# Optimization experiments

Hardware: AMD Instinct MI355X
Metric: run time of the kernel (lower is better)

The kernel has to match this reference:

```python
import jax, jax.numpy as jnp
import numpy as np

V, NB, NJ, NP, NK = 6890, 10, 24, 207, 19
PARENTS = np.array([-1, 0, 0, 0, 1, 2, 3, 4, 5, 6, 7, 8, 9, 9, 9, 12, 13, 14, 16, 17, 18, 19, 20, 21])


def setup_inputs():
    key = jax.random.key(0)
    ks = jax.random.split(key, 9)
    B = 1024
    beta = jax.random.normal(ks[0], (B, NB), jnp.float32)
    theta = jax.random.normal(ks[1], (B, NJ * 3), jnp.float32) * 0.3  # axis-angle per joint
    trans = jax.random.normal(ks[2], (B, 3), jnp.float32)
    v_template = jax.random.normal(ks[3], (V, 3), jnp.float32)
    shapedirs = jax.random.normal(ks[4], (NB, V * 3), jnp.float32) * 0.03
    Jr = jax.random.uniform(ks[5], (V, NJ), jnp.float32)
    J_regressor = Jr / jnp.sum(Jr, axis=0, keepdims=True)
    posedirs = jax.random.normal(ks[6], (NP, V * 3), jnp.float32) * 0.01
    jr = jax.random.uniform(ks[7], (V, NK), jnp.float32)
    joint_regressor = jr / jnp.sum(jr, axis=0, keepdims=True)
    w = jax.random.uniform(ks[8], (V, NJ), jnp.float32)
    weights = w / jnp.sum(w, axis=1, keepdims=True)  # LBS weights, rows sum to 1
    return dict(beta=beta, theta=theta, trans=trans, v_template=v_template,
                shapedirs=shapedirs, J_regressor=J_regressor, posedirs=posedirs,
                joint_regressor=joint_regressor, weights=weights)


def batch_rodrigues(theta):
    # theta: (N,3) axis-angle -> (N,3,3) rotation matrices via quaternions (HMR-style)
    angle = jnp.linalg.norm(theta + 1e-8, axis=1, keepdims=True)
    half = angle * 0.5
    v = (theta / angle) * jnp.sin(half)
    quat = jnp.concatenate([jnp.cos(half), v], axis=1)
    quat = quat / jnp.linalg.norm(quat, axis=1, keepdims=True)
    w, x, y, z = quat[:, 0], quat[:, 1], quat[:, 2], quat[:, 3]
    rot = jnp.stack([
        1 - 2 * (y * y + z * z), 2 * (x * y - w * z), 2 * (x * z + w * y),
        2 * (x * y + w * z), 1 - 2 * (x * x + z * z), 2 * (y * z - w * x),
        2 * (x * z - w * y), 2 * (y * z + w * x), 1 - 2 * (x * x + y * y)], axis=1)
    return rot.reshape(-1, 3, 3)


def batch_global_rigid_transformation(Rs, J):
    # Rs: (B,24,3,3), J: (B,24,3); rotate_base=True
    B = Rs.shape[0]
    rot_x = jnp.array([[1., 0., 0.], [0., -1., 0.], [0., 0., -1.]], jnp.float32)
    root_R = Rs[:, 0] @ rot_x

    def make_A(R, t):  # (B,3,3),(B,3) -> (B,4,4)
        top = jnp.concatenate([R, t[:, :, None]], axis=2)
        bot = jnp.broadcast_to(jnp.array([0., 0., 0., 1.], jnp.float32), (B, 1, 4))
        return jnp.concatenate([top, bot], axis=1)

    results = [make_A(root_R, J[:, 0])]
    for i in range(1, NJ):  # fixed 24-joint kinematic chain
        t = J[:, i] - J[:, PARENTS[i]]
        results.append(results[PARENTS[i]] @ make_A(Rs[:, i], t))
    res = jnp.stack(results, axis=1)  # (B,24,4,4)
    new_J = res[:, :, :3, 3]
    j_w0 = jnp.concatenate([J, jnp.zeros_like(J[:, :, :1])], axis=2)  # (B,24,4), homo w=0
    init_bone = jnp.einsum('bjrc,bjc->bjr', res, j_w0)
    A = res.at[:, :, :, 3].add(-init_bone)  # subtract only last column (matches F.pad trick)
    return new_J, A


def reference(beta, theta, trans, v_template, shapedirs, J_regressor, posedirs, joint_regressor, weights):
    B = beta.shape[0]
    v_shaped = (beta @ shapedirs).reshape(B, V, 3) + v_template
    J = jnp.einsum('bvc,vj->bjc', v_shaped, J_regressor)  # (B,24,3)
    Rs = batch_rodrigues(theta.reshape(-1, 3)).reshape(B, NJ, 3, 3)
    pose_feature = (Rs[:, 1:] - jnp.eye(3, dtype=Rs.dtype)).reshape(B, NP)
    v_posed = (pose_feature @ posedirs).reshape(B, V, 3) + v_shaped
    _, A = batch_global_rigid_transformation(Rs, J)
    T = jnp.einsum('vj,bjrc->bvrc', weights, A)  # (B,V,4,4) per-vertex skinning transforms
    homo = jnp.concatenate([v_posed, jnp.ones((B, V, 1), v_posed.dtype)], axis=2)
    verts = jnp.einsum('bvrc,bvc->bvr', T, homo)[:, :, :3] + trans[:, None, :]
    joints = jnp.einsum('bvc,vk->bkc', verts, joint_regressor)  # (B,19,3)
    return joints
```

## Files before the change

kernel.cpp:

```cpp
#include <hip/hip_runtime.h>
#include <hip/hip_bf16.h>

constexpr int Vn   = 6890;
constexpr int VC3  = 20670;
constexpr int NKB  = 216;
constexpr int QT   = 224;
constexpr int NMG  = 14;
constexpr int NCOL = 480;
constexpr int MC   = 1368;
constexpr int KCH  = 27;

using bf16x8  = __attribute__((ext_vector_type(8))) short;
using floatx4 = __attribute__((ext_vector_type(4))) float;

__device__ __forceinline__ unsigned short f2bf(float f) {
    unsigned int u = __float_as_uint(f);
    unsigned int r = (u + 0x7FFFu + ((u >> 16) & 1u)) >> 16;
    return (unsigned short)r;
}

__global__ __launch_bounds__(256) void k0_build(
    const float* __restrict__ vt, const float* __restrict__ sdirs,
    const float* __restrict__ pdirs, const float* __restrict__ Jreg,
    const float* __restrict__ jreg, const float* __restrict__ wts,
    unsigned short* __restrict__ Af, unsigned short* __restrict__ Bf)
{
    int bx = blockIdx.x, t = threadIdx.x;
    if (bx < 756) {
        int mg = bx / 54, ub = bx % 54;
        int ql = t & 15, q = mg * 16 + ql;
        int uu = ub * 16 + (t >> 4);
        int v0 = uu * 8, base = 3 * v0;
        float buf[24];
        if (q == 0) {
            #pragma unroll
            for (int i = 0; i < 24; ++i) buf[i] = (v0 + i / 3 < Vn) ? 1.f : 0.f;
        } else {
            const float* src = nullptr;
            if (q == 1) src = vt;
            else if (q >= 2 && q < 12)   src = sdirs + (size_t)(q - 2) * VC3;
            else if (q >= 12 && q < 219) src = pdirs + (size_t)(q - 12) * VC3;
            if (src && base + 23 < VC3) {
                #pragma unroll
                for (int i = 0; i < 12; ++i) {
                    float2 f = *(const float2*)(src + base + 2 * i);
                    buf[2 * i] = f.x; buf[2 * i + 1] = f.y;
                }
            } else {
                #pragma unroll
                for (int i = 0; i < 24; ++i)
                    buf[i] = (src && base + i < VC3) ? src[base + i] : 0.f;
            }
        }
        int kb = uu >> 2, quad = uu & 3;
        size_t foff = (size_t)(ql + quad * 16) * 8;
        #pragma unroll
        for (int c = 0; c < 3; ++c) {
            bf16x8 o;
            #pragma unroll
            for (int j = 0; j < 8; ++j) o[j] = (short)f2bf(buf[3 * j + c]);
            *(bf16x8*)(Af + ((size_t)(c * NMG + mg) * NKB + kb) * 512 + foff) = o;
        }
        return;
    }
    bx -= 756;
    {
        int v0 = bx * 64;
        __shared__ float js[64 * 19], wsh[64 * 24], Jsh[64 * 24];
        for (int i = t; i < 64 * 19; i += 256)
            js[i] = (v0 * 19 + i < Vn * 19) ? jreg[v0 * 19 + i] : 0.f;
        for (int i = t; i < 64 * 24; i += 256) {
            wsh[i] = (v0 * 24 + i < Vn * 24) ? wts[v0 * 24 + i] : 0.f;
            Jsh[i] = (v0 * 24 + i < Vn * 24) ? Jreg[v0 * 24 + i] : 0.f;
        }
        __syncthreads();
        for (int s = t; s < 4096; s += 256) {
            int clow = s & 15, w = s >> 4;
            int vg = w & 7, chigh = w >> 3;
            int col = chigh * 16 + clow;
            int kb = (v0 >> 5) + (vg >> 2);
            bf16x8 o;
            #pragma unroll
            for (int j = 0; j < 8; ++j) {
                int vl = vg * 8 + j;
                float val = 0.f;
                if (col < 456)      val = js[vl * 19 + col / 24] * wsh[vl * 24 + col % 24];
                else if (col < 480) val = Jsh[vl * 24 + (col - 456)];
                o[j] = (short)f2bf(val);
            }
            *(bf16x8*)(Bf + ((size_t)chigh * NKB + kb) * 512
                          + (size_t)(clow + (vg & 3) * 16) * 8) = o;
        }
    }
}

__device__ __forceinline__ void k1_load(bf16x8 (&a)[2], bf16x8 (&b)[4],
    const unsigned short* __restrict__ ap, const unsigned short* __restrict__ bp, int i)
{
    a[0] = *(const bf16x8*)(ap + (size_t)(0 * NKB + i) * 512);
    a[1] = *(const bf16x8*)(ap + (size_t)(1 * NKB + i) * 512);
    b[0] = *(const bf16x8*)(bp + (size_t)(0 * NKB + i) * 512);
    b[1] = *(const bf16x8*)(bp + (size_t)(1 * NKB + i) * 512);
    b[2] = *(const bf16x8*)(bp + (size_t)(2 * NKB + i) * 512);
    b[3] = *(const bf16x8*)(bp + (size_t)(3 * NKB + i) * 512);
}

__global__ __launch_bounds__(512) void k1_mfma(
    const unsigned short* __restrict__ Af, const unsigned short* __restrict__ Bf,
    unsigned short* __restrict__ Wb3, float* __restrict__ w1g,
    float* __restrict__ Jacc)
{
    __shared__ float red[8 * 2048];
    int tid = threadIdx.x;
    int wv = tid >> 6, l = tid & 63;
    int r = blockIdx.x;
    int c = r / 56; r %= 56;
    int mt = r >> 3, nt = r & 7;
    int kb0 = wv * KCH;

    const unsigned short* ap = Af + ((size_t)(c * NMG + mt * 2) * NKB + kb0) * 512 + l * 8;
    const unsigned short* bp = Bf + ((size_t)(nt * 4) * NKB + kb0) * 512 + l * 8;

    floatx4 acc[2][4];
    #pragma unroll
    for (int mi = 0; mi < 2; ++mi)
        #pragma unroll
        for (int ni = 0; ni < 4; ++ni) acc[mi][ni] = floatx4{0.f, 0.f, 0.f, 0.f};

    bf16x8 a[3][2], b[3][4];
    k1_load(a[0], b[0], ap, bp, 0);
    k1_load(a[1], b[1], ap, bp, 1);
    #pragma unroll
    for (int i = 0; i < KCH; ++i) {
        if (i + 2 < KCH) k1_load(a[(i + 2) % 3], b[(i + 2) % 3], ap, bp, i + 2);
        bf16x8 (&ac)[2] = a[i % 3];
        bf16x8 (&bc)[4] = b[i % 3];
        #pragma unroll
        for (int mi = 0; mi < 2; ++mi)
            #pragma unroll
            for (int ni = 0; ni < 4; ++ni)
                acc[mi][ni] = __builtin_amdgcn_mfma_f32_16x16x32_bf16(ac[mi], bc[ni], acc[mi][ni], 0, 0, 0);
    }
    #pragma unroll
    for (int mi = 0; mi < 2; ++mi)
        #pragma unroll
        for (int ni = 0; ni < 4; ++ni)
            *(floatx4*)&red[wv * 2048 + ((mi * 4 + ni) * 64 + l) * 4] = acc[mi][ni];
    __syncthreads();
    if (tid < 256) {
        int cl = tid & 63, qo = tid >> 6;
        int ni = cl >> 4;
        int q0 = qo * 8;
        int li0 = ((q0 & 15) >> 2) * 16 + (cl & 15);
        int li1 = (((q0 + 4) & 15) >> 2) * 16 + (cl & 15);
        int base0 = (((q0 >> 4) * 4 + ni) * 64 + li0) * 4;
        int base1 = ((((q0 + 4) >> 4) * 4 + ni) * 64 + li1) * 4;
        floatx4 s0{0.f, 0.f, 0.f, 0.f}, s1{0.f, 0.f, 0.f, 0.f};
        #pragma unroll
        for (int ww = 0; ww < 8; ++ww) {
            s0 += *(const floatx4*)&red[ww * 2048 + base0];
            s1 += *(const floatx4*)&red[ww * 2048 + base1];
        }
        int col = nt * 64 + cl;
        if (col < NCOL) {
            int colc = col * 3 + c;
            if (colc < MC) {
                bf16x8 o;
                #pragma unroll
                for (int j = 0; j < 4; ++j) {
                    o[j]     = (short)f2bf(s0[j]);
                    o[4 + j] = (short)f2bf(s1[j]);
                }
                *(bf16x8*)(Wb3 + ((size_t)(colc >> 4) * 7 + mt) * 512
                               + (size_t)((colc & 15) + qo * 16) * 8) = o;
            }
            if (c == 0 && mt == 0 && qo == 0 && col < 456) w1g[col] = s0[0];
            if (mt == 0 && col >= 456) {
                float* jb = Jacc + (size_t)((col - 456) * 3 + c) * 11;
                if (qo == 0) {
                    jb[0] = s0[1]; jb[1] = s0[2]; jb[2] = s0[3];
                    jb[3] = s1[0]; jb[4] = s1[1]; jb[5] = s1[2]; jb[6] = s1[3];
                } else if (qo == 1) {
                    jb[7] = s0[0]; jb[8] = s0[1]; jb[9] = s0[2]; jb[10] = s0[3];
                }
            }
        }
    }
}

__global__ __launch_bounds__(256) void k2a_prep(
    const float* __restrict__ Jacc, const float* __restrict__ beta,
    const float* __restrict__ theta,
    unsigned short* __restrict__ xbf, float* __restrict__ RAg, float* __restrict__ tAg)
{
    __shared__ float Rs[4][24][9];
    __shared__ float Jl[4][24][3];
    __shared__ float resR[4][24][9];
    __shared__ float rest_[4][24][3];
    __shared__ float bet[4][10];
    __shared__ float Jas[792];
    int t = threadIdx.x;
    int b0 = blockIdx.x * 4;

    if (t < 40) bet[t / 10][t % 10] = beta[(b0 + t / 10) * 10 + t % 10];
    for (int i = t; i < 792; i += 256) Jas[i] = Jacc[i];
    if (t >= 64 && t < 160) {
        int i = t - 64;
        int bl = i / 24, j = i % 24;
        float t0 = theta[(size_t)(b0 + bl) * 72 + j * 3 + 0];
        float t1 = theta[(size_t)(b0 + bl) * 72 + j * 3 + 1];
        float t2 = theta[(size_t)(b0 + bl) * 72 + j * 3 + 2];
        float e0 = t0 + 1e-8f, e1 = t1 + 1e-8f, e2 = t2 + 1e-8f;
        float angle = sqrtf(e0 * e0 + e1 * e1 + e2 * e2);
        float half = 0.5f * angle;
        float sh = sinf(half), ch = cosf(half);
        float s = sh / angle;
        float qx = t0 * s, qy = t1 * s, qz = t2 * s;
        float qn = sqrtf(ch * ch + qx * qx + qy * qy + qz * qz);
        float w = ch / qn, x = qx / qn, y = qy / qn, z = qz / qn;
        Rs[bl][j][0] = 1.f - 2.f * (y * y + z * z);
        Rs[bl][j][1] = 2.f * (x * y - w * z);
        Rs[bl][j][2] = 2.f * (x * z + w * y);
        Rs[bl][j][3] = 2.f * (x * y + w * z);
        Rs[bl][j][4] = 1.f - 2.f * (x * x + z * z);
        Rs[bl][j][5] = 2.f * (y * z - w * x);
        Rs[bl][j][6] = 2.f * (x * z - w * y);
        Rs[bl][j][7] = 2.f * (y * z + w * x);
        Rs[bl][j][8] = 1.f - 2.f * (x * x + y * y);
    }
    __syncthreads();
    for (int i = t; i < 4 * 72; i += 256) {
        int bl = i / 72, jc = i % 72;
        const float* bp_ = Jas + (size_t)jc * 11;
        float a = bp_[0];
        #pragma unroll
        for (int n = 0; n < 10; ++n) a += bet[bl][n] * bp_[1 + n];
        Jl[bl][jc / 3][jc % 3] = a;
    }
    for (int i = t; i < 4 * QT; i += 256) {
        int q = i >> 2, bl = i & 3;
        int b = b0 + bl;
        float xv = 0.f;
        if (q == 1) xv = 1.f;
        else if (q >= 2 && q < 12) xv = bet[bl][q - 2];
        else if (q >= 12 && q < 219) {
            int p = q - 12;
            int jj = 1 + p / 9, e = p % 9;
            float rr = Rs[bl][jj][e];
            if (e == 0 || e == 4 || e == 8) rr -= 1.f;
            xv = rr;
        }
        xbf[((size_t)(b >> 4) * 7 + (q >> 5)) * 512
            + (size_t)((b & 15) + ((q >> 3) & 3) * 16) * 8 + (q & 7)] = f2bf(xv);
    }
    __syncthreads();
    if (t < 12) {
        const int par[24] = {-1,0,0,0,1,2,3,4,5,6,7,8,9,9,9,12,13,14,16,17,18,19,20,21};
        int bl = t / 3, rr = t % 3;
        resR[bl][0][rr * 3 + 0] =  Rs[bl][0][rr * 3 + 0];
        resR[bl][0][rr * 3 + 1] = -Rs[bl][0][rr * 3 + 1];
        resR[bl][0][rr * 3 + 2] = -Rs[bl][0][rr * 3 + 2];
        rest_[bl][0][rr] = Jl[bl][0][rr];
        for (int i = 1; i < 24; ++i) {
            int p = par[i];
            float t0 = Jl[bl][i][0] - Jl[bl][p][0];
            float t1 = Jl[bl][i][1] - Jl[bl][p][1];
            float t2 = Jl[bl][i][2] - Jl[bl][p][2];
            float a0 = resR[bl][p][rr * 3 + 0], a1 = resR[bl][p][rr * 3 + 1],
                  a2 = resR[bl][p][rr * 3 + 2];
            resR[bl][i][rr * 3 + 0] = a0 * Rs[bl][i][0] + a1 * Rs[bl][i][3] + a2 * Rs[bl][i][6];
            resR[bl][i][rr * 3 + 1] = a0 * Rs[bl][i][1] + a1 * Rs[bl][i][4] + a2 * Rs[bl][i][7];
            resR[bl][i][rr * 3 + 2] = a0 * Rs[bl][i][2] + a1 * Rs[bl][i][5] + a2 * Rs[bl][i][8];
            rest_[bl][i][rr] = a0 * t0 + a1 * t1 + a2 * t2 + rest_[bl][p][rr];
        }
    }
    __syncthreads();
    for (int i = t; i < 4 * 216; i += 256) {
        int bl = i / 216, jr = i % 216;
        RAg[(size_t)(b0 + bl) * 216 + jr] = resR[bl][jr / 9][jr % 9];
    }
    for (int i = t; i < 4 * 72; i += 256) {
        int bl = i / 72, jc = i % 72;
        int j = jc / 3, c = jc % 3;
        tAg[(size_t)(b0 + bl) * 72 + jc] = rest_[bl][j][c]
            - (resR[bl][j][c * 3 + 0] * Jl[bl][j][0] + resR[bl][j][c * 3 + 1] * Jl[bl][j][1]
             + resR[bl][j][c * 3 + 2] * Jl[bl][j][2]);
    }
}

__global__ __launch_bounds__(256) void k2b_mfma(
    const unsigned short* __restrict__ Wb3, const unsigned short* __restrict__ xbf,
    float* __restrict__ Mg)
{
    int w = threadIdx.x >> 6, l = threadIdx.x & 63;
    int wm = w & 1, wn = w >> 1;
    int ct = blockIdx.x % 22, bt = blockIdx.x / 22;
    int mg0 = ct * 4 + wm * 2;
    int bg0 = bt * 8 + wn * 4;
    const unsigned short* ap = Wb3 + (size_t)mg0 * 7 * 512 + l * 8;
    const unsigned short* bp = xbf + (size_t)bg0 * 7 * 512 + l * 8;

    floatx4 acc[2][4];
    #pragma unroll
    for (int mi = 0; mi < 2; ++mi)
        #pragma unroll
        for (int ni = 0; ni < 4; ++ni) acc[mi][ni] = floatx4{0.f, 0.f, 0.f, 0.f};

    #pragma unroll
    for (int kk = 0; kk < 7; ++kk) {
        bf16x8 a0 = *(const bf16x8*)(ap + (size_t)(0 * 7 + kk) * 512);
        bf16x8 a1 = *(const bf16x8*)(ap + (size_t)(1 * 7 + kk) * 512);
        bf16x8 b0 = *(const bf16x8*)(bp + (size_t)(0 * 7 + kk) * 512);
        bf16x8 b1 = *(const bf16x8*)(bp + (size_t)(1 * 7 + kk) * 512);
        bf16x8 b2 = *(const bf16x8*)(bp + (size_t)(2 * 7 + kk) * 512);
        bf16x8 b3 = *(const bf16x8*)(bp + (size_t)(3 * 7 + kk) * 512);
        acc[0][0] = __builtin_amdgcn_mfma_f32_16x16x32_bf16(a0, b0, acc[0][0], 0, 0, 0);
        acc[0][1] = __builtin_amdgcn_mfma_f32_16x16x32_bf16(a0, b1, acc[0][1], 0, 0, 0);
        acc[0][2] = __builtin_amdgcn_mfma_f32_16x16x32_bf16(a0, b2, acc[0][2], 0, 0, 0);
        acc[0][3] = __builtin_amdgcn_mfma_f32_16x16x32_bf16(a0, b3, acc[0][3], 0, 0, 0);
        acc[1][0] = __builtin_amdgcn_mfma_f32_16x16x32_bf16(a1, b0, acc[1][0], 0, 0, 0);
        acc[1][1] = __builtin_amdgcn_mfma_f32_16x16x32_bf16(a1, b1, acc[1][1], 0, 0, 0);
        acc[1][2] = __builtin_amdgcn_mfma_f32_16x16x32_bf16(a1, b2, acc[1][2], 0, 0, 0);
        acc[1][3] = __builtin_amdgcn_mfma_f32_16x16x32_bf16(a1, b3, acc[1][3], 0, 0, 0);
    }
    int lr = l & 15, rq = (l >> 4) * 4;
    #pragma unroll
    for (int mi = 0; mi < 2; ++mi)
        #pragma unroll
        for (int ni = 0; ni < 4; ++ni) {
            int b  = bt * 128 + wn * 64 + ni * 16 + lr;
            int cc = (mg0 + mi) * 16 + rq;
            if (cc < MC)
                *(floatx4*)(Mg + (size_t)b * MC + cc) = acc[mi][ni];
        }
}

__global__ __launch_bounds__(256) void k2c_combine(
    const float* __restrict__ Mg, const float* __restrict__ RAg,
    const float* __restrict__ tAg, const float* __restrict__ w1g,
    const float* __restrict__ trans, float* __restrict__ out)
{
    __shared__ float w1s[456];
    __shared__ float Ms[4 * MC];
    __shared__ float RAs[4 * 216];
    __shared__ float tAs[4 * 72];
    int tid = threadIdx.x;
    int b0 = blockIdx.x * 4;
    for (int i = tid; i < 456; i += 256) w1s[i] = w1g[i];
    for (int i = tid; i < 4 * MC; i += 256) Ms[i] = Mg[(size_t)b0 * MC + i];
    for (int i = tid; i < 4 * 216; i += 256) RAs[i] = RAg[(size_t)b0 * 216 + i];
    for (int i = tid; i < 4 * 72; i += 256) tAs[i] = tAg[(size_t)b0 * 72 + i];
    __syncthreads();
    if (tid < 228) {
        int lb = tid / 57, kc = tid % 57;
        int k = kc / 3, c = kc % 3;
        int b = b0 + lb;
        float acc = trans[b * 3 + c];
        const float* Mrow = Ms + lb * MC;
        const float* RAr  = RAs + lb * 216;
        const float* tAr  = tAs + lb * 72;
        #pragma unroll
        for (int j = 0; j < 24; ++j) {
            int kj = k * 24 + j;
            float m0 = Mrow[kj * 3 + 0], m1 = Mrow[kj * 3 + 1], m2 = Mrow[kj * 3 + 2];
            acc += RAr[j * 9 + c * 3 + 0] * m0
                 + RAr[j * 9 + c * 3 + 1] * m1
                 + RAr[j * 9 + c * 3 + 2] * m2
                 + tAr[j * 3 + c] * w1s[kj];
        }
        out[b * 57 + kc] = acc;
    }
}

extern "C" void kernel_launch(void* const* d_in, const int* in_sizes, int n_in,
                              void* d_out, int out_size, void* d_ws, size_t ws_size,
                              hipStream_t stream)
{
    const float* beta  = (const float*)d_in[0];
    const float* theta = (const float*)d_in[1];
    const float* trans = (const float*)d_in[2];
    const float* vt    = (const float*)d_in[3];
    const float* sdirs = (const float*)d_in[4];
    const float* Jreg  = (const float*)d_in[5];
    const float* pdirs = (const float*)d_in[6];
    const float* jreg  = (const float*)d_in[7];
    const float* wts   = (const float*)d_in[8];
    float* out = (float*)d_out;
    int B = in_sizes[0] / 10;

    unsigned short* Af  = (unsigned short*)d_ws;
    unsigned short* Bf  = Af + (size_t)42 * NKB * 512;
    unsigned short* Wb3 = Bf + (size_t)32 * NKB * 512;
    unsigned short* xbf = Wb3 + (size_t)88 * 7 * 512;
    float* Jacc = (float*)(xbf + (size_t)64 * 7 * 512);
    float* w1g  = Jacc + 792;
    float* RAg  = w1g + 456;
    float* tAg  = RAg + (size_t)B * 216;
    float* Mg   = tAg + (size_t)B * 72;

    k0_build<<<dim3(756 + 108), 256, 0, stream>>>(
        vt, sdirs, pdirs, Jreg, jreg, wts, Af, Bf);
    k1_mfma<<<dim3(168), 512, 0, stream>>>(Af, Bf, Wb3, w1g, Jacc);
    k2a_prep<<<dim3(B / 4), 256, 0, stream>>>(
        Jacc, beta, theta, xbf, RAg, tAg);
    k2b_mfma<<<dim3((B / 128) * 22), 256, 0, stream>>>(Wb3, xbf, Mg);
    k2c_combine<<<dim3(B / 4), 256, 0, stream>>>(Mg, RAg, tAg, w1g, trans, out);
}
```

Baseline: 134.2 us.

## Fuse combine stage into MFMA epilogue with atomic accumulation into output

Removes the separate combine kernel and the intermediate M buffer (B x 1368 floats). The translation and bias part of the output is now written by the prep kernel, and the MFMA kernel's epilogue multiplies its accumulators by the per-batch rotation entries and atomically adds partial sums into the output. This saves one launch and a global round-trip of the M matrix. In exchange it adds many scattered float atomics, and the result now depends on prep finishing its writes before the MFMA kernel runs, which stream order provides.

```diff
diff --git a/kernel.cpp b/kernel.cpp
--- a/kernel.cpp
+++ b/kernel.cpp
@@ -190,20 +190,25 @@
 
 __global__ __launch_bounds__(256) void k2a_prep(
     const float* __restrict__ Jacc, const float* __restrict__ beta,
-    const float* __restrict__ theta,
-    unsigned short* __restrict__ xbf, float* __restrict__ RAg, float* __restrict__ tAg)
+    const float* __restrict__ theta, const float* __restrict__ w1g,
+    const float* __restrict__ trans,
+    unsigned short* __restrict__ xbf, float* __restrict__ RAg,
+    float* __restrict__ out)
 {
     __shared__ float Rs[4][24][9];
     __shared__ float Jl[4][24][3];
     __shared__ float resR[4][24][9];
     __shared__ float rest_[4][24][3];
+    __shared__ float tAs[4][72];
     __shared__ float bet[4][10];
     __shared__ float Jas[792];
+    __shared__ float w1s[456];
     int t = threadIdx.x;
     int b0 = blockIdx.x * 4;
 
     if (t < 40) bet[t / 10][t % 10] = beta[(b0 + t / 10) * 10 + t % 10];
     for (int i = t; i < 792; i += 256) Jas[i] = Jacc[i];
+    for (int i = t; i < 456; i += 256) w1s[i] = w1g[i];
     if (t >= 64 && t < 160) {
         int i = t - 64;
         int bl = i / 24, j = i % 24;
@@ -282,15 +287,27 @@
     for (int i = t; i < 4 * 72; i += 256) {
         int bl = i / 72, jc = i % 72;
         int j = jc / 3, c = jc % 3;
-        tAg[(size_t)(b0 + bl) * 72 + jc] = rest_[bl][j][c]
+        tAs[bl][jc] = rest_[bl][j][c]
             - (resR[bl][j][c * 3 + 0] * Jl[bl][j][0] + resR[bl][j][c * 3 + 1] * Jl[bl][j][1]
              + resR[bl][j][c * 3 + 2] * Jl[bl][j][2]);
     }
+    __syncthreads();
+    for (int i = t; i < 4 * 57; i += 256) {
+        int lb = i / 57, kc = i % 57;
+        int k = kc / 3, c = kc % 3;
+        int b = b0 + lb;
+        float acc = trans[b * 3 + c];
+        const float* tAr = tAs[lb];
+        #pragma unroll
+        for (int j = 0; j < 24; ++j)
+            acc += tAr[j * 3 + c] * w1s[k * 24 + j];
+        out[b * 57 + kc] = acc;
+    }
 }
 
 __global__ __launch_bounds__(256) void k2b_mfma(
     const unsigned short* __restrict__ Wb3, const unsigned short* __restrict__ xbf,
-    float* __restrict__ Mg)
+    const float* __restrict__ RAg, float* __restrict__ out)
 {
     int w = threadIdx.x >> 6, l = threadIdx.x & 63;
     int wm = w & 1, wn = w >> 1;
@@ -325,50 +342,42 @@
     }
     int lr = l & 15, rq = (l >> 4) * 4;
     #pragma unroll
-    for (int mi = 0; mi < 2; ++mi)
+    for (int mi = 0; mi < 2; ++mi) {
+        int ccb = (mg0 + mi) * 16 + rq;
         #pragma unroll
         for (int ni = 0; ni < 4; ++ni) {
-            int b  = bt * 128 + wn * 64 + ni * 16 + lr;
-            int cc = (mg0 + mi) * 16 + rq;
-            if (cc < MC)
-                *(floatx4*)(Mg + (size_t)b * MC + cc) = acc[mi][ni];
-        }
-}
-
-__global__ __launch_bounds__(256) void k2c_combine(
-    const float* __restrict__ Mg, const float* __restrict__ RAg,
-    const float* __restrict__ tAg, const float* __restrict__ w1g,
-    const float* __restrict__ trans, float* __restrict__ out)
-{
-    __shared__ float w1s[456];
-    __shared__ float Ms[4 * MC];
-    __shared__ float RAs[4 * 216];
-    __shared__ float tAs[4 * 72];
-    int tid = threadIdx.x;
-    int b0 = blockIdx.x * 4;
-    for (int i = tid; i < 456; i += 256) w1s[i] = w1g[i];
-    for (int i = tid; i < 4 * MC; i += 256) Ms[i] = Mg[(size_t)b0 * MC + i];
-    for (int i = tid; i < 4 * 216; i += 256) RAs[i] = RAg[(size_t)b0 * 216 + i];
-    for (int i = tid; i < 4 * 72; i += 256) tAs[i] = tAg[(size_t)b0 * 72 + i];
-    __syncthreads();
-    if (tid < 228) {
-        int lb = tid / 57, kc = tid % 57;
-        int k = kc / 3, c = kc % 3;
-        int b = b0 + lb;
-        float acc = trans[b * 3 + c];
-        const float* Mrow = Ms + lb * MC;
-        const float* RAr  = RAs + lb * 216;
-        const float* tAr  = tAs + lb * 72;
-        #pragma unroll
-        for (int j = 0; j < 24; ++j) {
-            int kj = k * 24 + j;
-            float m0 = Mrow[kj * 3 + 0], m1 = Mrow[kj * 3 + 1], m2 = Mrow[kj * 3 + 2];
-            acc += RAr[j * 9 + c * 3 + 0] * m0
-                 + RAr[j * 9 + c * 3 + 1] * m1
-                 + RAr[j * 9 + c * 3 + 2] * m2
-                 + tAr[j * 3 + c] * w1s[kj];
-        }
-        out[b * 57 + kc] = acc;
+            int b = bt * 128 + wn * 64 + ni * 16 + lr;
+            float* ob = out + (size_t)b * 57;
+            const float* RAb = RAg + (size_t)b * 216;
+            int prevk = -1;
+            float s0 = 0.f, s1 = 0.f, s2 = 0.f;
+            #pragma unroll
+            for (int rr = 0; rr < 4; ++rr) {
+                int cc = ccb + rr;
+                if (cc < MC) {
+                    int kj = cc / 3, cm = cc - kj * 3;
+                    int k = kj / 24, j = kj - k * 24;
+                    float m = acc[mi][ni][rr];
+                    const float* ra = RAb + j * 9 + cm;
+                    if (k != prevk) {
+                        if (prevk >= 0) {
+                            atomicAdd(&ob[prevk * 3 + 0], s0);
+                            atomicAdd(&ob[prevk * 3 + 1], s1);
+                            atomicAdd(&ob[prevk * 3 + 2], s2);
+                        }
+                        prevk = k; s0 = s1 = s2 = 0.f;
+                    }
+                    s0 += ra[0] * m;
+                    s1 += ra[3] * m;
+                    s2 += ra[6] * m;
+                }
+            }
+            if (prevk >= 0) {
+                atomicAdd(&ob[prevk * 3 + 0], s0);
+                atomicAdd(&ob[prevk * 3 + 1], s1);
+                atomicAdd(&ob[prevk * 3 + 2], s2);
+            }
+        }
     }
 }
 
@@ -395,14 +404,11 @@
     float* Jacc = (float*)(xbf + (size_t)64 * 7 * 512);
     float* w1g  = Jacc + 792;
     float* RAg  = w1g + 456;
-    float* tAg  = RAg + (size_t)B * 216;
-    float* Mg   = tAg + (size_t)B * 72;
 
     k0_build<<<dim3(756 + 108), 256, 0, stream>>>(
         vt, sdirs, pdirs, Jreg, jreg, wts, Af, Bf);
     k1_mfma<<<dim3(168), 512, 0, stream>>>(Af, Bf, Wb3, w1g, Jacc);
     k2a_prep<<<dim3(B / 4), 256, 0, stream>>>(
-        Jacc, beta, theta, xbf, RAg, tAg);
-    k2b_mfma<<<dim3((B / 128) * 22), 256, 0, stream>>>(Wb3, xbf, Mg);
-    k2c_combine<<<dim3(B / 4), 256, 0, stream>>>(Mg, RAg, tAg, w1g, trans, out);
-}
+        Jacc, beta, theta, w1g, trans, xbf, RAg, out);
+    k2b_mfma<<<dim3((B / 128) * 22), 256, 0, stream>>>(Wb3, xbf, RAg, out);
+}
```

Result: slower. 197.7 us (+47.3%).
